# Kernel tuning notes

Hardware: AMD Instinct MI355X
Metric: run time of the kernel (lower is better)

## Reference

```python
import jax, jax.numpy as jnp
import numpy as np

# Conv2d_mvm config (matches init_kwargs): the bit-sliced crossbar MVM is a
# fixed-point emulation of an exact stride-1 conv2d with padding=1, no bias.
C_IN, C_OUT, K, H, W, PAD = 16, 16, 3, 1024, 1024, 1


def setup_inputs() -> dict:
    key = jax.random.key(0)
    kx, kw = jax.random.split(key)
    x = jax.random.normal(kx, (1, C_IN, H, W), dtype=jnp.float32)
    # kaiming_uniform-style init for the conv weight
    fan_in = C_IN * K * K
    bound = 1.0 / np.sqrt(fan_in)
    weight = jax.random.uniform(kw, (C_OUT, C_IN, K, K), dtype=jnp.float32,
                                minval=-bound, maxval=bound)
    return {"x": x, "weight": weight}


def reference(x, weight):
    # Ideal math of the bit-sliced crossbar MVM: per output pixel, the
    # flattened (C_in*K*K) receptive field dotted with each flattened filter.
    out = jax.lax.conv_general_dilated(
        x, weight,
        window_strides=(1, 1),
        padding=((PAD, PAD), (PAD, PAD)),
        dimension_numbers=("NCHW", "OIHW", "NCHW"),
    )
    # Original forward returns (C_out, H_out, W_out) with batch=1 assumed.
    return out[0]
```

## Files before the change

### kernel.cpp

```cpp
#include <hip/hip_runtime.h>


#define H 1024
#define W 1024
#define HW (H * W)
#define TW 128
#define TH 8
#define LROWS 10
#define NQ 34
#define NJOBS (LROWS * NQ)
#define LCOLS 130
#define LPITCH (LCOLS * 32)
#define LDS_BYTES (LROWS * LPITCH)

typedef __bf16 bf16x8 __attribute__((ext_vector_type(8)));
typedef float f32x4 __attribute__((ext_vector_type(4)));
typedef unsigned short ushort8 __attribute__((ext_vector_type(8)));
typedef unsigned int uint4v __attribute__((ext_vector_type(4)));

__device__ __host__ inline unsigned short f2bf(float f) {
  unsigned u = __builtin_bit_cast(unsigned, f);
  return (unsigned short)((u + 0x7fffu + ((u >> 16) & 1u)) >> 16);
}

__global__ __launch_bounds__(256) void conv_prep(const float* __restrict__ w,
                                                 unsigned short* __restrict__ wA) {
  int i = blockIdx.x * 256 + threadIdx.x;
  if (i >= 5 * 64 * 8) return;
  int j = i & 7;
  int l = (i >> 3) & 63;
  int p = i >> 9;
  int k = (l >> 4) * 8 + j;
  int t = 2 * p + (k >> 4);
  int ci = k & 15;
  int co = l & 15;
  float v = (t <= 8) ? w[co * 144 + ci * 9 + t] : 0.f;
  wA[i] = f2bf(v);
}

__device__ __forceinline__ void stage_job(int j, const float* __restrict__ x,
                                          int colbase, int rowbase, char* lds) {
  const int ly  = j / NQ;
  const int qx  = j - ly * NQ;
  const int gy  = rowbase - 1 + ly;
  const float rowm = ((unsigned)gy < (unsigned)H) ? 1.f : 0.f;
  const int gyc  = gy < 0 ? 0 : (gy > H - 1 ? H - 1 : gy);
  const int gx0  = colbase - 4 + 4 * qx;
  const int gx0c = gx0 < 0 ? 0 : (gx0 > W - 4 ? W - 4 : gx0);
  const float* xb = x + gyc * W + gx0c;

  f32x4 L[16];
#pragma unroll
  for (int c = 0; c < 16; ++c)
    L[c] = *(const f32x4*)(xb + c * HW);

#pragma unroll
  for (int i = 0; i < 4; ++i) {
    const int gx = gx0 + i;
    const int lx = gx - (colbase - 1);
    if ((unsigned)lx < (unsigned)LCOLS) {
      const float fm = rowm * (((unsigned)gx < (unsigned)W) ? 1.f : 0.f);
      const int lb = (ly * LPITCH + lx * 32) ^ (((lx >> 2) & 3) << 4);
#pragma unroll
      for (int h = 0; h < 2; ++h) {
        uint4v d;
#pragma unroll
        for (int p = 0; p < 4; ++p) {
          const unsigned lo = f2bf(L[h * 8 + 2 * p][i] * fm);
          const unsigned hi = f2bf(L[h * 8 + 2 * p + 1][i] * fm);
          d[p] = lo | (hi << 16);
        }
        *(uint4v*)(lds + (lb ^ (h << 4))) = d;
      }
    }
  }
}

__global__ __launch_bounds__(256, 3) void conv_mfma(
    const float* __restrict__ x, const unsigned short* __restrict__ wA,
    float* __restrict__ out) {
  __shared__ __align__(16) char lds[LDS_BYTES];

  const int tid  = threadIdx.x;
  const int lane = tid & 63;
  const int wave = tid >> 6;
  const int m = lane & 15;
  const int q = lane >> 4;
  const int colbase = blockIdx.x * TW;
  const int rowbase = blockIdx.y * TH;

  stage_job(tid, x, colbase, rowbase, lds);
  if (tid < NJOBS - 256) stage_job(256 + tid, x, colbase, rowbase, lds);

  ushort8 wU[5];
#pragma unroll
  for (int p = 0; p < 5; ++p)
    wU[p] = *(const ushort8*)&wA[(p * 64 + lane) * 8];

  int baseaddr[5];
#pragma unroll
  for (int p = 0; p < 5; ++p) {
    int t = 2 * p + (q >> 1);
    int ky = 0, kx = 0;
    if (t <= 8) { ky = t / 3; kx = t - ky * 3; }
    int col = m + kx;
    int b = ky * LPITCH + col * 32 + (q & 1) * 16;
    b ^= ((col >> 2) & 3) << 4;
    baseaddr[p] = b + wave * 2 * LPITCH;
  }

  __syncthreads();

#pragma unroll
  for (int r = 0; r < 2; ++r) {
#pragma unroll
    for (int g = 0; g < 8; ++g) {
      f32x4 acc = {0.f, 0.f, 0.f, 0.f};
#pragma unroll
      for (int p = 0; p < 5; ++p) {
        ushort8 bU = *(const ushort8*)(lds + (baseaddr[p] + r * LPITCH + g * 512));
        acc = __builtin_amdgcn_mfma_f32_16x16x32_bf16(
            __builtin_bit_cast(bf16x8, bU),
            __builtin_bit_cast(bf16x8, wU[p]),
            acc, 0, 0, 0);
      }
      const int y  = rowbase + wave * 2 + r;
      const int x0 = colbase + g * 16 + q * 4;
      *(f32x4*)(out + m * HW + y * W + x0) = acc;
    }
  }
}

extern "C" void kernel_launch(void* const* d_in, const int* in_sizes, int n_in,
                              void* d_out, int out_size, void* d_ws, size_t ws_size,
                              hipStream_t stream) {
  const float* x = (const float*)d_in[0];
  const float* w = (const float*)d_in[1];
  float* out = (float*)d_out;
  unsigned short* wA = (unsigned short*)d_ws;

  conv_prep<<<10, 256, 0, stream>>>(w, wA);

  dim3 grid(W / TW, H / TH);
  conv_mfma<<<grid, 256, 0, stream>>>(x, wA, out);
}
```

Before: 39.49 us.

## Fuse weight prep into conv kernel and batch input loads via inline asm

```diff
diff --git a/kernel.cpp b/kernel.cpp
--- a/kernel.cpp
+++ b/kernel.cpp
@@ -23,21 +23,6 @@
   return (unsigned short)((u + 0x7fffu + ((u >> 16) & 1u)) >> 16);
 }
 
-__global__ __launch_bounds__(256) void conv_prep(const float* __restrict__ w,
-                                                 unsigned short* __restrict__ wA) {
-  int i = blockIdx.x * 256 + threadIdx.x;
-  if (i >= 5 * 64 * 8) return;
-  int j = i & 7;
-  int l = (i >> 3) & 63;
-  int p = i >> 9;
-  int k = (l >> 4) * 8 + j;
-  int t = 2 * p + (k >> 4);
-  int ci = k & 15;
-  int co = l & 15;
-  float v = (t <= 8) ? w[co * 144 + ci * 9 + t] : 0.f;
-  wA[i] = f2bf(v);
-}
-
 __device__ __forceinline__ void stage_job(int j, const float* __restrict__ x,
                                           int colbase, int rowbase, char* lds) {
   const int ly  = j / NQ;
@@ -47,12 +32,39 @@
   const int gyc  = gy < 0 ? 0 : (gy > H - 1 ? H - 1 : gy);
   const int gx0  = colbase - 4 + 4 * qx;
   const int gx0c = gx0 < 0 ? 0 : (gx0 > W - 4 ? W - 4 : gx0);
-  const float* xb = x + gyc * W + gx0c;
+  const unsigned voff = (unsigned)((gyc * W + gx0c) * 4);
 
   f32x4 L[16];
-#pragma unroll
-  for (int c = 0; c < 16; ++c)
-    L[c] = *(const f32x4*)(xb + c * HW);
+  asm volatile(
+      "global_load_dwordx4 %0, %8, %9\n\t"
+      "global_load_dwordx4 %1, %8, %10\n\t"
+      "global_load_dwordx4 %2, %8, %11\n\t"
+      "global_load_dwordx4 %3, %8, %12\n\t"
+      "global_load_dwordx4 %4, %8, %13\n\t"
+      "global_load_dwordx4 %5, %8, %14\n\t"
+      "global_load_dwordx4 %6, %8, %15\n\t"
+      "global_load_dwordx4 %7, %8, %16\n\t"
+      : "=&v"(L[0]), "=&v"(L[1]), "=&v"(L[2]), "=&v"(L[3]),
+        "=&v"(L[4]), "=&v"(L[5]), "=&v"(L[6]), "=&v"(L[7])
+      : "v"(voff), "s"(x), "s"(x + HW), "s"(x + 2 * HW), "s"(x + 3 * HW),
+        "s"(x + 4 * HW), "s"(x + 5 * HW), "s"(x + 6 * HW), "s"(x + 7 * HW));
+  asm volatile(
+      "global_load_dwordx4 %0, %8, %9\n\t"
+      "global_load_dwordx4 %1, %8, %10\n\t"
+      "global_load_dwordx4 %2, %8, %11\n\t"
+      "global_load_dwordx4 %3, %8, %12\n\t"
+      "global_load_dwordx4 %4, %8, %13\n\t"
+      "global_load_dwordx4 %5, %8, %14\n\t"
+      "global_load_dwordx4 %6, %8, %15\n\t"
+      "global_load_dwordx4 %7, %8, %16\n\t"
+      : "=&v"(L[8]), "=&v"(L[9]), "=&v"(L[10]), "=&v"(L[11]),
+        "=&v"(L[12]), "=&v"(L[13]), "=&v"(L[14]), "=&v"(L[15])
+      : "v"(voff), "s"(x + 8 * HW), "s"(x + 9 * HW), "s"(x + 10 * HW),
+        "s"(x + 11 * HW), "s"(x + 12 * HW), "s"(x + 13 * HW),
+        "s"(x + 14 * HW), "s"(x + 15 * HW));
+
+  asm volatile("s_waitcnt vmcnt(0)" ::: "memory");
+  __builtin_amdgcn_sched_barrier(0);
 
 #pragma unroll
   for (int i = 0; i < 4; ++i) {
@@ -76,8 +88,8 @@
   }
 }
 
-__global__ __launch_bounds__(256, 3) void conv_mfma(
-    const float* __restrict__ x, const unsigned short* __restrict__ wA,
+__global__ __launch_bounds__(256) void conv_mfma(
+    const float* __restrict__ x, const float* __restrict__ w,
     float* __restrict__ out) {
   __shared__ __align__(16) char lds[LDS_BYTES];
 
@@ -93,9 +105,20 @@
   if (tid < NJOBS - 256) stage_job(256 + tid, x, colbase, rowbase, lds);
 
   ushort8 wU[5];
+  {
+    const int tq = q >> 1, ci0 = (q & 1) * 8;
 #pragma unroll
-  for (int p = 0; p < 5; ++p)
-    wU[p] = *(const ushort8*)&wA[(p * 64 + lane) * 8];
+    for (int p = 0; p < 5; ++p) {
+      const int t = 2 * p + tq;
+      ushort8 u;
+#pragma unroll
+      for (int j = 0; j < 8; ++j) {
+        float v = (t <= 8) ? w[m * 144 + (ci0 + j) * 9 + t] : 0.f;
+        u[j] = f2bf(v);
+      }
+      wU[p] = u;
+    }
+  }
 
   int baseaddr[5];
 #pragma unroll
@@ -137,10 +160,7 @@
   const float* x = (const float*)d_in[0];
   const float* w = (const float*)d_in[1];
   float* out = (float*)d_out;
-  unsigned short* wA = (unsigned short*)d_ws;
-
-  conv_prep<<<10, 256, 0, stream>>>(w, wA);
 
   dim3 grid(W / TW, H / TH);
-  conv_mfma<<<grid, 256, 0, stream>>>(x, wA, out);
+  conv_mfma<<<grid, 256, 0, stream>>>(x, w, out);
 }
```

New measurement: 42.11 us. 6.6% more time.
